# Kernel tuning notes

Measured on AMD Instinct MI355X. Metric: run time of the kernel, lower is better.

The kernel has to match this reference:

```python
import jax, jax.numpy as jnp
import numpy as np

N_NODES = 100000
N_HIDDEN = 128
N_EDGES = 625000
EPS = 1e-12  # F.normalize default eps


def setup_inputs() -> dict:
    key = jax.random.key(0)
    k1, k2, k3 = jax.random.split(key, 3)
    emb = jax.random.normal(k1, (N_NODES, N_HIDDEN), dtype=jnp.float32)
    edge_src = jax.random.randint(k2, (N_EDGES,), 0, N_NODES, dtype=jnp.int64)
    edge_dst = jax.random.randint(k3, (N_EDGES,), 0, N_NODES, dtype=jnp.int64)
    d = jnp.ones((N_HIDDEN,), dtype=jnp.float32)
    scale = jnp.ones((1,), dtype=jnp.float32)
    return {"emb": emb, "edge_src": edge_src, "edge_dst": edge_dst, "d": d, "scale": scale}


def reference(emb, edge_src, edge_dst, d, scale):
    # L2 normalize rows (torch F.normalize: x / max(||x||, eps))
    norm = jnp.linalg.norm(emb, axis=1, keepdims=True)
    e = emb / jnp.maximum(norm, EPS)            # [N, H]
    ew = e * d                                  # diag scale, [N, H]
    # edge-wise u_dot_v: sum over feature dim of ew[src] * e[dst]
    z = jnp.sum(ew[edge_src] * e[edge_dst], axis=1, keepdims=True)  # [E, 1]
    return z * scale
```

## Files before the change

kernel.cpp:

```cpp
#include <hip/hip_runtime.h>

#define NORM_EPS 1e-12f

#if defined(__has_builtin) && __has_builtin(__builtin_amdgcn_sdot4)
__device__ __forceinline__ int sdot4(unsigned a, unsigned b, int c) {
    return __builtin_amdgcn_sdot4((int)a, (int)b, c, false);
}
#else
__device__ __forceinline__ int sdot4(unsigned a, unsigned b, int c) {
    #pragma unroll
    for (int i = 0; i < 4; ++i)
        c += (int)(signed char)(a >> (8 * i)) * (int)(signed char)(b >> (8 * i));
    return c;
}
#endif

__global__ void build_tables_kernel(const float* __restrict__ emb,
                                    const float* __restrict__ dvec,
                                    unsigned short* __restrict__ tblE,
                                    unsigned short* __restrict__ tblW,
                                    float* __restrict__ scl,
                                    int* __restrict__ flag,
                                    int n_nodes) {
    int row  = (blockIdx.x * blockDim.x + threadIdx.x) >> 6;
    int lane = threadIdx.x & 63;
    if (row >= n_nodes) return;

    const float2* p = (const float2*)(emb + (size_t)row * 128);
    float2 v = p[lane];
    float s = v.x * v.x + v.y * v.y;
    #pragma unroll
    for (int off = 32; off > 0; off >>= 1)
        s += __shfl_xor(s, off);
    float inv = 1.0f / fmaxf(sqrtf(s), NORM_EPS);

    float2 d2 = ((const float2*)dvec)[lane];
    bool neg_lane = (d2.x < 0.0f) || (d2.y < 0.0f);
    int has_neg = (__ballot(neg_lane) != 0ull) ? 1 : 0;

    float r0 = sqrtf(fabsf(d2.x)), r1 = sqrtf(fabsf(d2.y));
    float e0 = v.x * inv * r0, e1 = v.y * inv * r1;

    float m = fmaxf(fabsf(e0), fabsf(e1));
    #pragma unroll
    for (int off = 32; off > 0; off >>= 1)
        m = fmaxf(m, __shfl_xor(m, off));

    float q = (m > 0.f) ? 127.0f / m : 0.f;
    int qe0 = __float2int_rn(e0 * q), qe1 = __float2int_rn(e1 * q);
    tblE[(size_t)row * 64 + lane] =
        (unsigned short)((qe0 & 0xFF) | ((qe1 & 0xFF) << 8));

    if (has_neg) {
        float w0 = (d2.x < 0.0f) ? -e0 : e0;
        float w1 = (d2.y < 0.0f) ? -e1 : e1;
        int qw0 = __float2int_rn(w0 * q), qw1 = __float2int_rn(w1 * q);
        tblW[(size_t)row * 64 + lane] =
            (unsigned short)((qw0 & 0xFF) | ((qw1 & 0xFF) << 8));
    }
    if (lane == 0) {
        scl[row] = m * (1.0f / 127.0f);
        if (row == 0) flag[0] = has_neg;
    }
}

__global__ void edge_dot_i8_kernel(const uint4* __restrict__ tE,
                                   const uint4* __restrict__ tW,
                                   const float* __restrict__ scl,
                                   const int* __restrict__ flag,
                                   const int* __restrict__ esrc,
                                   const int* __restrict__ edst,
                                   const float* __restrict__ scale,
                                   float* __restrict__ out,
                                   int n_edges) {
    int g    = (blockIdx.x * blockDim.x + threadIdx.x) >> 3;
    int lane = threadIdx.x & 7;
    int e0 = g * 2, e1 = e0 + 1;
    if (e0 >= n_edges) return;
    bool has1 = e1 < n_edges;

    const uint4* tS = (flag[0] != 0) ? tW : tE;

    int s0 = esrc[e0], t0 = edst[e0];
    int s1 = has1 ? esrc[e1] : s0;
    int t1 = has1 ? edst[e1] : t0;

    uint4 a0 = tS[(size_t)s0 * 8 + lane];
    uint4 b0 = tE[(size_t)t0 * 8 + lane];
    uint4 a1 = tS[(size_t)s1 * 8 + lane];
    uint4 b1 = tE[(size_t)t1 * 8 + lane];

    float ss0 = scl[s0] * scl[t0];
    float ss1 = scl[s1] * scl[t1];

    int i0 = 0, i1 = 0;
    i0 = sdot4(a0.x, b0.x, i0); i0 = sdot4(a0.y, b0.y, i0);
    i0 = sdot4(a0.z, b0.z, i0); i0 = sdot4(a0.w, b0.w, i0);
    i1 = sdot4(a1.x, b1.x, i1); i1 = sdot4(a1.y, b1.y, i1);
    i1 = sdot4(a1.z, b1.z, i1); i1 = sdot4(a1.w, b1.w, i1);

    #pragma unroll
    for (int off = 4; off > 0; off >>= 1) {
        i0 += __shfl_xor(i0, off);
        i1 += __shfl_xor(i1, off);
    }

    if (lane == 0) {
        float sc = scale[0];
        out[e0] = (float)i0 * ss0 * sc;
        if (has1) out[e1] = (float)i1 * ss1 * sc;
    }
}

extern "C" void kernel_launch(void* const* d_in, const int* in_sizes, int n_in,
                              void* d_out, int out_size, void* d_ws, size_t ws_size,
                              hipStream_t stream) {
    const float* emb   = (const float*)d_in[0];
    const int*   esrc  = (const int*)d_in[1];
    const int*   edst  = (const int*)d_in[2];
    const float* dvec  = (const float*)d_in[3];
    const float* scale = (const float*)d_in[4];
    float*       out   = (float*)d_out;

    int n_nodes = in_sizes[0] / 128;
    int n_edges = in_sizes[1];

    char* base = (char*)d_ws;
    size_t tbl_bytes = (size_t)n_nodes * 128;
    unsigned short* tblE = (unsigned short*)base;
    unsigned short* tblW = (unsigned short*)(base + tbl_bytes);
    float*          scl  = (float*)(base + 2 * tbl_bytes);
    int*            flag = (int*)(base + 2 * tbl_bytes + (size_t)n_nodes * 4);

    {
        int blocks = (n_nodes + 3) / 4;
        build_tables_kernel<<<blocks, 256, 0, stream>>>(
            emb, dvec, tblE, tblW, scl, flag, n_nodes);
    }
    {
        int n_groups = (n_edges + 1) / 2;
        long long threads = (long long)n_groups * 8;
        int blocks = (int)((threads + 255) / 256);
        edge_dot_i8_kernel<<<blocks, 256, 0, stream>>>(
            (const uint4*)tblE, (const uint4*)tblW, scl, flag,
            esrc, edst, scale, out, n_edges);
    }
}
```

Baseline: 126.0 us.

## Process eight edges per 8-lane group and halve waves in table build

The edge kernel now gives each lane one edge. The lane loads its own indices and scales coalesced, broadcasts them within the 8-lane group with shuffles, and runs eight gathered int8 dot products. A transpose-style butterfly reduction then leaves each lane holding its own edge's sum, so every lane writes one output instead of one lane per edge. The table build packs two rows per wave with float4 loads and 32-bit packed stores. The aim is fewer index loads and scalar stores and fewer wasted lanes, at the cost of more registers and shuffle work per thread.

```diff
diff --git a/kernel.cpp b/kernel.cpp
--- a/kernel.cpp
+++ b/kernel.cpp
@@ -15,101 +15,121 @@
 }
 #endif
 
-__global__ void build_tables_kernel(const float* __restrict__ emb,
-                                    const float* __restrict__ dvec,
-                                    unsigned short* __restrict__ tblE,
-                                    unsigned short* __restrict__ tblW,
-                                    float* __restrict__ scl,
-                                    int* __restrict__ flag,
-                                    int n_nodes) {
-    int row  = (blockIdx.x * blockDim.x + threadIdx.x) >> 6;
+__global__ __launch_bounds__(256) void build_tables_kernel(
+        const float* __restrict__ emb,
+        const float* __restrict__ dvec,
+        unsigned* __restrict__ tblE,
+        unsigned* __restrict__ tblW,
+        float* __restrict__ scl,
+        int* __restrict__ flag,
+        int n_nodes) {
+    int wid  = (blockIdx.x * blockDim.x + threadIdx.x) >> 6;
     int lane = threadIdx.x & 63;
-    if (row >= n_nodes) return;
+    int r    = lane & 31;
+    int row  = wid * 2 + (lane >> 5);
+    bool valid = row < n_nodes;
+    int crow = valid ? row : (n_nodes - 1);
 
-    const float2* p = (const float2*)(emb + (size_t)row * 128);
-    float2 v = p[lane];
-    float s = v.x * v.x + v.y * v.y;
+    float4 v = ((const float4*)(emb + (size_t)crow * 128))[r];
+    float s = v.x * v.x + v.y * v.y + v.z * v.z + v.w * v.w;
     #pragma unroll
-    for (int off = 32; off > 0; off >>= 1)
+    for (int off = 16; off > 0; off >>= 1)
         s += __shfl_xor(s, off);
     float inv = 1.0f / fmaxf(sqrtf(s), NORM_EPS);
 
-    float2 d2 = ((const float2*)dvec)[lane];
-    bool neg_lane = (d2.x < 0.0f) || (d2.y < 0.0f);
+    float4 d4 = ((const float4*)dvec)[r];
+    bool neg_lane = (d4.x < 0.f) || (d4.y < 0.f) || (d4.z < 0.f) || (d4.w < 0.f);
     int has_neg = (__ballot(neg_lane) != 0ull) ? 1 : 0;
 
-    float r0 = sqrtf(fabsf(d2.x)), r1 = sqrtf(fabsf(d2.y));
-    float e0 = v.x * inv * r0, e1 = v.y * inv * r1;
+    float e0 = v.x * inv * sqrtf(fabsf(d4.x));
+    float e1 = v.y * inv * sqrtf(fabsf(d4.y));
+    float e2 = v.z * inv * sqrtf(fabsf(d4.z));
+    float e3 = v.w * inv * sqrtf(fabsf(d4.w));
 
-    float m = fmaxf(fabsf(e0), fabsf(e1));
+    float m = fmaxf(fmaxf(fabsf(e0), fabsf(e1)), fmaxf(fabsf(e2), fabsf(e3)));
     #pragma unroll
-    for (int off = 32; off > 0; off >>= 1)
+    for (int off = 16; off > 0; off >>= 1)
         m = fmaxf(m, __shfl_xor(m, off));
 
     float q = (m > 0.f) ? 127.0f / m : 0.f;
-    int qe0 = __float2int_rn(e0 * q), qe1 = __float2int_rn(e1 * q);
-    tblE[(size_t)row * 64 + lane] =
-        (unsigned short)((qe0 & 0xFF) | ((qe1 & 0xFF) << 8));
+    int q0 = __float2int_rn(e0 * q), q1 = __float2int_rn(e1 * q);
+    int q2 = __float2int_rn(e2 * q), q3 = __float2int_rn(e3 * q);
+    unsigned pk = (unsigned)(q0 & 0xFF) | ((unsigned)(q1 & 0xFF) << 8) |
+                  ((unsigned)(q2 & 0xFF) << 16) | ((unsigned)(q3 & 0xFF) << 24);
+    if (valid) tblE[(size_t)crow * 32 + r] = pk;
 
     if (has_neg) {
-        float w0 = (d2.x < 0.0f) ? -e0 : e0;
-        float w1 = (d2.y < 0.0f) ? -e1 : e1;
-        int qw0 = __float2int_rn(w0 * q), qw1 = __float2int_rn(w1 * q);
-        tblW[(size_t)row * 64 + lane] =
-            (unsigned short)((qw0 & 0xFF) | ((qw1 & 0xFF) << 8));
+        float w0 = (d4.x < 0.f) ? -e0 : e0;
+        float w1 = (d4.y < 0.f) ? -e1 : e1;
+        float w2 = (d4.z < 0.f) ? -e2 : e2;
+        float w3 = (d4.w < 0.f) ? -e3 : e3;
+        int p0 = __float2int_rn(w0 * q), p1 = __float2int_rn(w1 * q);
+        int p2 = __float2int_rn(w2 * q), p3 = __float2int_rn(w3 * q);
+        unsigned pw = (unsigned)(p0 & 0xFF) | ((unsigned)(p1 & 0xFF) << 8) |
+                      ((unsigned)(p2 & 0xFF) << 16) | ((unsigned)(p3 & 0xFF) << 24);
+        if (valid) tblW[(size_t)crow * 32 + r] = pw;
     }
-    if (lane == 0) {
-        scl[row] = m * (1.0f / 127.0f);
-        if (row == 0) flag[0] = has_neg;
+    if (valid && r == 0) {
+        scl[crow] = m * (1.0f / 127.0f);
+        if (crow == 0) flag[0] = has_neg;
     }
 }
 
-__global__ void edge_dot_i8_kernel(const uint4* __restrict__ tE,
-                                   const uint4* __restrict__ tW,
-                                   const float* __restrict__ scl,
-                                   const int* __restrict__ flag,
-                                   const int* __restrict__ esrc,
-                                   const int* __restrict__ edst,
-                                   const float* __restrict__ scale,
-                                   float* __restrict__ out,
-                                   int n_edges) {
-    int g    = (blockIdx.x * blockDim.x + threadIdx.x) >> 3;
-    int lane = threadIdx.x & 7;
-    int e0 = g * 2, e1 = e0 + 1;
-    if (e0 >= n_edges) return;
-    bool has1 = e1 < n_edges;
+__global__ __launch_bounds__(256) void edge_dot_i8_kernel(
+        const uint4* __restrict__ tE,
+        const uint4* __restrict__ tW,
+        const float* __restrict__ scl,
+        const int* __restrict__ flag,
+        const int* __restrict__ esrc,
+        const int* __restrict__ edst,
+        const float* __restrict__ scale,
+        float* __restrict__ out,
+        int n_edges) {
+    long long gtid = (long long)blockIdx.x * blockDim.x + threadIdx.x;
+    int lane8 = threadIdx.x & 7;
+    long long base = gtid - lane8;
+    if (base >= n_edges) return;
+    bool valid = gtid < n_edges;
+    int e = valid ? (int)gtid : (n_edges - 1);
+
+    int s_own = esrc[e];
+    int t_own = edst[e];
+    float ss = scl[s_own] * scl[t_own];
 
     const uint4* tS = (flag[0] != 0) ? tW : tE;
 
-    int s0 = esrc[e0], t0 = edst[e0];
-    int s1 = has1 ? esrc[e1] : s0;
-    int t1 = has1 ? edst[e1] : t0;
-
-    uint4 a0 = tS[(size_t)s0 * 8 + lane];
-    uint4 b0 = tE[(size_t)t0 * 8 + lane];
-    uint4 a1 = tS[(size_t)s1 * 8 + lane];
-    uint4 b1 = tE[(size_t)t1 * 8 + lane];
-
-    float ss0 = scl[s0] * scl[t0];
-    float ss1 = scl[s1] * scl[t1];
-
-    int i0 = 0, i1 = 0;
-    i0 = sdot4(a0.x, b0.x, i0); i0 = sdot4(a0.y, b0.y, i0);
-    i0 = sdot4(a0.z, b0.z, i0); i0 = sdot4(a0.w, b0.w, i0);
-    i1 = sdot4(a1.x, b1.x, i1); i1 = sdot4(a1.y, b1.y, i1);
-    i1 = sdot4(a1.z, b1.z, i1); i1 = sdot4(a1.w, b1.w, i1);
-
+    int v[8];
     #pragma unroll
-    for (int off = 4; off > 0; off >>= 1) {
-        i0 += __shfl_xor(i0, off);
-        i1 += __shfl_xor(i1, off);
+    for (int k = 0; k < 8; ++k) {
+        int rs = __shfl(s_own, k, 8);
+        int rt = __shfl(t_own, k, 8);
+        uint4 a = tS[(size_t)rs * 8 + lane8];
+        uint4 b = tE[(size_t)rt * 8 + lane8];
+        int acc = 0;
+        acc = sdot4(a.x, b.x, acc); acc = sdot4(a.y, b.y, acc);
+        acc = sdot4(a.z, b.z, acc); acc = sdot4(a.w, b.w, acc);
+        v[k] = acc;
     }
 
-    if (lane == 0) {
-        float sc = scale[0];
-        out[e0] = (float)i0 * ss0 * sc;
-        if (has1) out[e1] = (float)i1 * ss1 * sc;
-    }
+    int k0, s0;
+    k0 = (lane8 & 1) ? v[1] : v[0];  s0 = (lane8 & 1) ? v[0] : v[1];
+    int w0 = k0 + __shfl_xor(s0, 1);
+    k0 = (lane8 & 1) ? v[3] : v[2];  s0 = (lane8 & 1) ? v[2] : v[3];
+    int w1 = k0 + __shfl_xor(s0, 1);
+    k0 = (lane8 & 1) ? v[5] : v[4];  s0 = (lane8 & 1) ? v[4] : v[5];
+    int w2 = k0 + __shfl_xor(s0, 1);
+    k0 = (lane8 & 1) ? v[7] : v[6];  s0 = (lane8 & 1) ? v[6] : v[7];
+    int w3 = k0 + __shfl_xor(s0, 1);
+
+    k0 = (lane8 & 2) ? w1 : w0;  s0 = (lane8 & 2) ? w0 : w1;
+    int u0 = k0 + __shfl_xor(s0, 2);
+    k0 = (lane8 & 2) ? w3 : w2;  s0 = (lane8 & 2) ? w2 : w3;
+    int u1 = k0 + __shfl_xor(s0, 2);
+
+    k0 = (lane8 & 4) ? u1 : u0;  s0 = (lane8 & 4) ? u0 : u1;
+    int tot = k0 + __shfl_xor(s0, 4);
+
+    if (valid) out[gtid] = (float)tot * ss * scale[0];
 }
 
 extern "C" void kernel_launch(void* const* d_in, const int* in_sizes, int n_in,
@@ -127,19 +147,19 @@
 
     char* base = (char*)d_ws;
     size_t tbl_bytes = (size_t)n_nodes * 128;
-    unsigned short* tblE = (unsigned short*)base;
-    unsigned short* tblW = (unsigned short*)(base + tbl_bytes);
-    float*          scl  = (float*)(base + 2 * tbl_bytes);
-    int*            flag = (int*)(base + 2 * tbl_bytes + (size_t)n_nodes * 4);
+    unsigned* tblE = (unsigned*)base;
+    unsigned* tblW = (unsigned*)(base + tbl_bytes);
+    float*    scl  = (float*)(base + 2 * tbl_bytes);
+    int*      flag = (int*)(base + 2 * tbl_bytes + (size_t)n_nodes * 4);
 
     {
-        int blocks = (n_nodes + 3) / 4;
+        int waves  = (n_nodes + 1) / 2;
+        int blocks = (waves + 3) / 4;
         build_tables_kernel<<<blocks, 256, 0, stream>>>(
             emb, dvec, tblE, tblW, scl, flag, n_nodes);
     }
     {
-        int n_groups = (n_edges + 1) / 2;
-        long long threads = (long long)n_groups * 8;
+        long long threads = ((long long)n_edges + 7) / 8 * 8;
         int blocks = (int)((threads + 255) / 256);
         edge_dot_i8_kernel<<<blocks, 256, 0, stream>>>(
             (const uint4*)tblE, (const uint4*)tblW, scl, flag,
```

New measurement: 117.5 us. 1.07x faster.
